# Kernel optimization log

Hardware: AMD Instinct MI355X
Metric: run time of the kernel (lower is better)

## Reference

```python
import jax, jax.numpy as jnp
import numpy as np

B, N, IN, E, H, F = 64, 256, 128, 256, 8, 1024


def setup_inputs() -> dict:
    key = jax.random.key(0)
    ks = jax.random.split(key, 16)
    x = jax.random.normal(ks[0], (B, N, IN), jnp.float32)
    adj = (jax.random.uniform(ks[1], (B, N, N)) < 0.1).astype(jnp.float32)
    adj = jnp.maximum(adj, adj.transpose(0, 2, 1))  # symmetric 0/1 adjacency
    mask = jax.random.randint(ks[2], (B, N), 0, 2).astype(jnp.float32)
    dist = jax.random.normal(ks[3], (B, N, N), jnp.float32)

    def lin(k, i, o):
        return (jax.random.normal(k, (i, o), jnp.float32) / np.sqrt(i)).astype(jnp.float32)

    return dict(
        x=x, adj=adj, mask=mask, dist=dist,
        W1=lin(ks[4], IN, E), b1=jnp.zeros((E,), jnp.float32),
        W2=lin(ks[5], E, E), b2=jnp.zeros((E,), jnp.float32),
        W3=lin(ks[6], E, E), b3=jnp.zeros((E,), jnp.float32),
        ln1_g=jnp.ones((E,), jnp.float32), ln1_b=jnp.zeros((E,), jnp.float32),
        Wq=lin(ks[7], E, H * E), Wk=lin(ks[8], E, H * E), Wv=lin(ks[9], E, H * E),
        Wo=lin(ks[10], H * E, E), bo=jnp.zeros((E,), jnp.float32),
        ln2_g=jnp.ones((E,), jnp.float32), ln2_b=jnp.zeros((E,), jnp.float32),
        Wf1=lin(ks[11], E, F), bf1=jnp.zeros((F,), jnp.float32),
        Wf2=lin(ks[12], F, E), bf2=jnp.zeros((E,), jnp.float32),
    )


def _layernorm(x, g, b):
    m = x.mean(-1, keepdims=True)
    v = ((x - m) ** 2).mean(-1, keepdims=True)
    return (x - m) * jax.lax.rsqrt(v + 1e-5) * g + b


def reference(x, adj, mask, dist, W1, b1, W2, b2, W3, b3, ln1_g, ln1_b,
              Wq, Wk, Wv, Wo, bo, ln2_g, ln2_b, Wf1, bf1, Wf2, bf2):
    # --- DenseGCNConv normalization (add self-loops, sym-normalize) ---
    eye = jnp.eye(N, dtype=adj.dtype)
    A = adj * (1.0 - eye) + eye                      # fill_diag(adj, 1)
    dis = jax.lax.rsqrt(jnp.clip(A.sum(-1), 1.0, None))
    An = dis[:, :, None] * A * dis[:, None, :]       # D^-1/2 A D^-1/2, [B,N,N]
    m3 = mask[:, :, None]

    def gcn(h, W, b):
        return (jnp.einsum('bij,bjf->bif', An, h @ W) + b) * m3

    g1 = jax.nn.relu(gcn(x, W1, b1))
    g2 = jax.nn.relu(gcn(g1, W2, b2))
    g3 = jax.nn.relu(gcn(g2, W3, b3))
    gcn_res = g1 + g2 + g3

    # --- masked MHA with distance bias (head dim = E per head) ---
    h = _layernorm(gcn_res, ln1_g, ln1_b)
    mh = mask[:, None, :, None]                      # [B,1,N,1]
    q = (h @ Wq).reshape(B, N, H, E).transpose(0, 2, 1, 3) * mh
    k = (h @ Wk).reshape(B, N, H, E).transpose(0, 2, 1, 3) * mh
    v = (h @ Wv).reshape(B, N, H, E).transpose(0, 2, 1, 3) * mh
    a = jnp.einsum('bhne,bhme->bhnm', q * (E ** -0.5), k) + dist[:, None]
    am = (mask[:, :, None] * mask[:, None, :])[:, None]  # [B,1,N,N]
    a = jnp.where(am == 0, -1e9, a)
    a = jax.nn.softmax(a, axis=-1)
    a = jnp.where(am == 0, 0.0, a)
    y = jnp.einsum('bhnm,bhme->bhne', a, v).transpose(0, 2, 1, 3).reshape(B, N, H * E)
    y = (y @ Wo + bo) * m3
    att = gcn_res + y

    # --- FFN block ---
    f = _layernorm(att, ln2_g, ln2_b)
    f = (jax.nn.gelu(f @ Wf1 + bf1, approximate=False) @ Wf2 + bf2) * m3
    att = att + f
    return gcn_res + att
```

## Files before the change

kernel.cpp:

```cpp
#include <hip/hip_runtime.h>
#include <hip/hip_bf16.h>
#include <cmath>

#define BB 64
#define NNODES 256
#define INF_ 128
#define EE 256
#define HH 8
#define FFN 1024
#define BNROWS 16384

typedef __attribute__((ext_vector_type(8))) short short8;
typedef __attribute__((ext_vector_type(4))) float floatx4;
typedef __attribute__((ext_vector_type(4))) unsigned short ushort4v;

__device__ __forceinline__ float b2f(unsigned short u) {
  union { unsigned u32; float f; } w; w.u32 = ((unsigned)u) << 16; return w.f;
}
__device__ __forceinline__ unsigned short f2b(float f) {
  union { float f; unsigned u32; } w; w.f = f;
  unsigned r = w.u32 + 0x7FFFu + ((w.u32 >> 16) & 1u);
  return (unsigned short)(r >> 16);
}
__device__ __forceinline__ float gelu_f(float x) {
  const float z = 0.7978845608028654f * (x + 0.044715f * x * x * x);
  const float e = __expf(2.0f * z);
  const float th = (e - 1.0f) / (e + 1.0f);
  return 0.5f * x * (1.0f + th);
}

typedef const __attribute__((address_space(1))) void GV;
typedef __attribute__((address_space(3))) void LV;

__device__ __forceinline__ void gl_lds16(const unsigned short* g,
                                         unsigned short* l, int lane) {
#if __has_builtin(__builtin_amdgcn_global_load_lds)
  __builtin_amdgcn_global_load_lds((GV*)g, (LV*)l, 16, 0, 0);
#else
  *(short8*)(l + lane * 8) = *(const short8*)g;
#endif
}

struct PackArgs {
  const float* src[12];
  unsigned short* dst[12];
  int R[12], C[12];
  int start[13];
};

__launch_bounds__(256)
__global__ void pack_kernel(PackArgs a)
{
  __shared__ float tile[32][33];
  const int bid = blockIdx.x;
  int j = 0;
  while (bid >= a.start[j + 1]) j++;
  const int lb = bid - a.start[j];
  const float* src = a.src[j];
  unsigned short* dst = a.dst[j];
  const int R = a.R[j], C = a.C[j];

  if (C == 0) {
    const int i = (lb * 256 + threadIdx.x) * 4;
    if (i >= R) return;
    floatx4 v = *(const floatx4*)(src + i);
    ushort4v o;
    #pragma unroll
    for (int k = 0; k < 4; k++) o[k] = f2b(v[k]);
    *(ushort4v*)(dst + i) = o;
    return;
  }
  const int tpr = C >> 5;
  const int c0 = (lb % tpr) * 32, r0 = (lb / tpr) * 32;
  const int tx = threadIdx.x & 31, ty = threadIdx.x >> 5;
  #pragma unroll
  for (int i = ty; i < 32; i += 8)
    tile[i][tx] = src[(long long)(r0 + i) * C + c0 + tx];
  __syncthreads();
  #pragma unroll
  for (int i = ty; i < 32; i += 8)
    dst[(long long)(c0 + i) * R + r0 + tx] = f2b(tile[tx][i]);
}

__global__ void deg_kernel(const float* __restrict__ adj,
                           float* __restrict__ dis)
{
  const int g = blockIdx.x * 4 + (threadIdx.x >> 6);
  const int lane = threadIdx.x & 63;
  const int i = g & 255;
  floatx4 v = *(const floatx4*)(adj + (long long)g * 256 + lane * 4);
  float s = 0.f;
  #pragma unroll
  for (int jj = 0; jj < 4; jj++) {
    const int j = lane * 4 + jj;
    s += (j == i) ? 1.0f : v[jj];
  }
  #pragma unroll
  for (int off = 32; off > 0; off >>= 1) s += __shfl_xor(s, off);
  if (lane == 0) dis[g] = 1.0f / sqrtf(fmaxf(s, 1.0f));
}

__global__ void an_kernel(const float* __restrict__ adj,
                          const float* __restrict__ dis,
                          unsigned short* __restrict__ An)
{
  const long long base = ((long long)blockIdx.x * 256 + threadIdx.x) * 4;
  const int rowg = (int)(base >> 8);
  const int i = rowg & 255;
  const int brow = rowg & ~255;
  const int j0 = (int)(base & 255);
  const float di = dis[rowg];
  floatx4 v = *(const floatx4*)(adj + base);
  ushort4v o;
  #pragma unroll
  for (int jj = 0; jj < 4; jj++) {
    const int j = j0 + jj;
    const float a = (j == i) ? 1.0f : v[jj];
    o[jj] = f2b(di * dis[brow + j] * a);
  }
  *(ushort4v*)(An + base) = o;
}

__launch_bounds__(512, 4)
__global__ void gemm_kernel(const unsigned short* __restrict__ A, int lda,
                            long long sAo, long long sAi,
                            const unsigned short* __restrict__ Bm, int ldb,
                            long long sBo, long long sBi,
                            void* __restrict__ Cv, int ldc,
                            long long sCo, long long sCi,
                            int K, int zshift, int mode, int flag,
                            const float* __restrict__ aux1,
                            const float* __restrict__ mask,
                            float* __restrict__ gcn,
                            void* __restrict__ aux2)
{
  __shared__ __align__(16) unsigned short sA[16384];
  __shared__ __align__(16) unsigned short sB[16384];

  const int t = threadIdx.x;
  const int z = blockIdx.z;
  const int zi = z & ((1 << zshift) - 1);
  const int zb = z >> zshift;
  const int m0 = blockIdx.x * 128;
  const int n0 = blockIdx.y * 128;
  A  += zb * sAo + zi * sAi;
  Bm += zb * sBo + zi * sBi;
  const long long cbase = zb * sCo + zi * sCi;

  const int lane = t & 63;
  const int w = t >> 6;
  const int wm = w >> 2, wn = w & 3;
  const int lm = lane & 15, qd = lane >> 4;

  floatx4 acc[4][2] = {};

  const int sub = lane >> 4;
  const int qs  = lane & 15;
  const unsigned short* pA[4];
  const unsigned short* pB[4];
  #pragma unroll
  for (int i = 0; i < 4; i++) {
    const int d = w * 4 + i;
    const int r = d * 4 + sub;
    const int co = (qs ^ (r & 7)) * 8;
    pA[i] = A + (long long)(m0 + r) * lda + co;
    pB[i] = Bm + (long long)(n0 + r) * ldb + co;
  }

  for (int kk = 0; kk < K; kk += 128) {
    #pragma unroll
    for (int i = 0; i < 4; i++) {
      gl_lds16(pA[i] + kk, &sA[(w * 4 + i) * 512], lane);
      gl_lds16(pB[i] + kk, &sB[(w * 4 + i) * 512], lane);
    }
    __syncthreads();

    #pragma unroll
    for (int ks = 0; ks < 4; ks++) {
      short8 af[4], bg[2];
      const int q = ks * 4 + qd;
      #pragma unroll
      for (int mi = 0; mi < 4; mi++) {
        const int r = wm * 64 + mi * 16 + lm;
        af[mi] = *(const short8*)&sA[r * 128 + ((q ^ (r & 7)) * 8)];
      }
      #pragma unroll
      for (int ni = 0; ni < 2; ni++) {
        const int r = wn * 32 + ni * 16 + lm;
        bg[ni] = *(const short8*)&sB[r * 128 + ((q ^ (r & 7)) * 8)];
      }
      #pragma unroll
      for (int mi = 0; mi < 4; mi++)
        #pragma unroll
        for (int ni = 0; ni < 2; ni++)
          acc[mi][ni] = __builtin_amdgcn_mfma_f32_16x16x32_bf16(
              af[mi], bg[ni], acc[mi][ni], 0, 0, 0);
    }
    __syncthreads();
  }

  #pragma unroll
  for (int mi = 0; mi < 4; mi++) {
    const int row0 = m0 + wm * 64 + mi * 16 + qd * 4;
    #pragma unroll
    for (int ni = 0; ni < 2; ni++) {
      const int col = n0 + wn * 32 + ni * 16 + lm;
      floatx4 a = acc[mi][ni];
      if (mode == 0) {
        float* Cf = (float*)Cv;
        #pragma unroll
        for (int r = 0; r < 4; r++)
          Cf[cbase + (long long)(row0 + r) * ldc + col] = a[r];
      } else if (mode == 1) {
        unsigned short* Cb = (unsigned short*)Cv;
        #pragma unroll
        for (int r = 0; r < 4; r++)
          Cb[cbase + (long long)(row0 + r) * ldc + col] = f2b(a[r]);
      } else if (mode == 2) {
        float* Cf = (float*)Cv;
        #pragma unroll
        for (int r = 0; r < 4; r++)
          Cf[cbase + (long long)(row0 + r) * ldc + col] += a[r];
      } else if (mode == 3) {
        unsigned short* Cb = (unsigned short*)Cv;
        const float bv = aux1[col];
        #pragma unroll
        for (int r = 0; r < 4; r++)
          Cb[cbase + (long long)(row0 + r) * ldc + col] = f2b(gelu_f(a[r] + bv));
      } else if (mode == 5) {
        const int b = row0 >> 8, n = row0 & 255;
        ushort4v o;
        #pragma unroll
        for (int r = 0; r < 4; r++) o[r] = f2b(a[r]);
        *(ushort4v*)((unsigned short*)Cv + (long long)b * 65536 + col * 256 + n) = o;
      } else if (mode == 8) {
        float* Cf = (float*)Cv;
        const float* attf = (const float*)aux2;
        const float bv = aux1[col];
        #pragma unroll
        for (int r = 0; r < 4; r++) {
          const long long idx = (long long)(row0 + r) * 256 + col;
          Cf[idx] = gcn[idx] + attf[idx] + (a[r] + bv) * mask[row0 + r];
        }
      } else if (mode == 9) {
        const int token = zb * 256 + col;
        const float m = mask[token];
        ushort4v o; floatx4 g;
        #pragma unroll
        for (int r = 0; r < 4; r++) {
          const float v = fmaxf((a[r] + aux1[row0 + r]) * m, 0.f);
          o[r] = f2b(v); g[r] = v;
        }
        *(ushort4v*)((unsigned short*)Cv + (long long)token * 256 + row0) = o;
        float* gp = gcn + (long long)token * 256 + row0;
        if (flag) { floatx4 old = *(const floatx4*)gp; g += old; }
        *(floatx4*)gp = g;
      } else if (mode == 12) {
        float* Cf = (float*)Cv;
        const float bv = aux1[col];
        #pragma unroll
        for (int r = 0; r < 4; r++) {
          const long long idx = (long long)(row0 + r) * 256 + col;
          Cf[idx] = gcn[idx] + (a[r] + bv) * mask[row0 + r];
        }
      } else if (mode == 13) {
        unsigned short* Cb = (unsigned short*)Cv;
        #pragma unroll
        for (int r = 0; r < 4; r++)
          Cb[cbase + (long long)(row0 + r) * ldc + col] = f2b(a[r] * 0.0625f);
      } else {
        if (col < 2048) {
          unsigned short* Cb = (unsigned short*)Cv;
          #pragma unroll
          for (int r = 0; r < 4; r++)
            Cb[(long long)(row0 + r) * 2048 + col] = f2b(a[r]);
        } else {
          const int z2 = (row0 >> 8) * 8 + ((col >> 8) - 8);
          const int e = col & 255, n = row0 & 255;
          ushort4v o;
          #pragma unroll
          for (int r = 0; r < 4; r++) o[r] = f2b(a[r]);
          *(ushort4v*)((unsigned short*)aux2 + (long long)z2 * 65536 + e * 256 + n) = o;
        }
      }
    }
  }
}

__launch_bounds__(512, 2)
__global__ void attn_kernel(unsigned short* __restrict__ QP,
                            const unsigned short* __restrict__ HBF,
                            const unsigned short* __restrict__ VT,
                            const unsigned short* __restrict__ DSTB,
                            const float* __restrict__ mask)
{
  __shared__ __align__(16) unsigned short sP[32768];
  __shared__ __align__(16) unsigned short sKV[32768];
  __shared__ float redm[2][128];
  __shared__ float reds[2][128];

  const int bi = blockIdx.x;
  const int x = bi & 7, sdx = bi >> 3;
  const int h = sdx & 7;
  const int p = (sdx >> 3) * 8 + x;
  const int b = p >> 1, mt = p & 1;
  const int m0 = mt * 128;
  const int z = b * 8 + h;

  const int t = threadIdx.x, lane = t & 63, w = t >> 6;
  const int lm = lane & 15, qd = lane >> 4;
  const int wm4 = w >> 1, wn2 = w & 1;
  const int wmP = w >> 2, wnP = w & 3;

  unsigned short* Qm = QP + ((long long)(b * 256 + m0)) * 2048 + h * 256;
  const unsigned short* Hb = HBF + (long long)b * 65536;
  const unsigned short* Vb = VT + (long long)z * 65536;
  const unsigned short* db = DSTB + (long long)b * 65536;
  const float* maskb = mask + b * 256;

  const int rin2 = lane >> 5, qs32 = lane & 31;
  const int rin8 = lane >> 3, qs8  = lane & 7;

  #pragma unroll
  for (int i = 0; i < 8; i++) {
    const int d = w * 8 + i;
    const int r = d * 2 + rin2;
    gl_lds16(Qm + (long long)r * 2048 + ((qs32 ^ (r & 7)) * 8), &sP[d * 512], lane);
  }
  #pragma unroll
  for (int i = 0; i < 4; i++) {
    const int d = w * 4 + i;
    const int r = d * 2 + rin2;
    gl_lds16(Hb + (long long)r * 256 + ((qs32 ^ (r & 7)) * 8), &sKV[d * 512], lane);
  }
  __syncthreads();

  short8 afq[2][8];
  #pragma unroll
  for (int mi = 0; mi < 2; mi++) {
    const int r = wm4 * 32 + mi * 16 + lm;
    #pragma unroll
    for (int ks = 0; ks < 8; ks++) {
      const int q = ks * 4 + qd;
      afq[mi][ks] = *(const short8*)&sP[r * 256 + ((q ^ (r & 7)) * 8)];
    }
  }

  floatx4 S[4][2][2] = {};
  #pragma unroll
  for (int c = 0; c < 4; c++) {
    const int cur = (c & 1) * 16384;
    if (c < 3) {
      #pragma unroll
      for (int i = 0; i < 4; i++) {
        const int d = w * 4 + i;
        const int r = d * 2 + rin2;
        gl_lds16(Hb + (long long)((c + 1) * 64 + r) * 256 + ((qs32 ^ (r & 7)) * 8),
                 &sKV[(cur ^ 16384) + d * 512], lane);
      }
    }
    #pragma unroll
    for (int ks = 0; ks < 8; ks++) {
      const int q = ks * 4 + qd;
      short8 bg[2];
      #pragma unroll
      for (int ni = 0; ni < 2; ni++) {
        const int kk = wn2 * 32 + ni * 16 + lm;
        bg[ni] = *(const short8*)&sKV[cur + kk * 256 + ((q ^ (kk & 7)) * 8)];
      }
      #pragma unroll
      for (int mi = 0; mi < 2; mi++)
        #pragma unroll
        for (int ni = 0; ni < 2; ni++)
          S[c][mi][ni] = __builtin_amdgcn_mfma_f32_16x16x32_bf16(
              afq[mi][ks], bg[ni], S[c][mi][ni], 0, 0, 0);
    }
    __syncthreads();
  }

  #pragma unroll
  for (int i = 0; i < 4; i++) {
    const int d = w * 4 + i;
    const int r = d * 8 + rin8;
    gl_lds16(Vb + (long long)r * 256 + ((qs8 ^ (r & 7)) * 8), &sKV[d * 512], lane);
  }

  float mkv[4][2];
  #pragma unroll
  for (int c = 0; c < 4; c++)
    #pragma unroll
    for (int ni = 0; ni < 2; ni++)
      mkv[c][ni] = maskb[c * 64 + wn2 * 32 + ni * 16 + lm];

  float lred[2][4];
  #pragma unroll
  for (int mi = 0; mi < 2; mi++) {
    #pragma unroll
    for (int r = 0; r < 4; r++) {
      const int row = wm4 * 32 + mi * 16 + qd * 4 + r;
      const float mq = maskb[m0 + row];
      float mx = -3e38f;
      #pragma unroll
      for (int c = 0; c < 4; c++)
        #pragma unroll
        for (int ni = 0; ni < 2; ni++) {
          const int col = c * 64 + wn2 * 32 + ni * 16 + lm;
          const float dv = b2f(db[(long long)(m0 + row) * 256 + col]);
          const float v = (mq != 0.f && mkv[c][ni] != 0.f) ? (S[c][mi][ni][r] + dv) : -1e9f;
          S[c][mi][ni][r] = v;
          mx = fmaxf(mx, v);
        }
      lred[mi][r] = mx;
    }
  }
  #pragma unroll
  for (int off = 1; off < 16; off <<= 1)
    #pragma unroll
    for (int mi = 0; mi < 2; mi++)
      #pragma unroll
      for (int r = 0; r < 4; r++)
        lred[mi][r] = fmaxf(lred[mi][r], __shfl_xor(lred[mi][r], off));
  if (lm == 0)
    #pragma unroll
    for (int mi = 0; mi < 2; mi++)
      #pragma unroll
      for (int r = 0; r < 4; r++)
        redm[wn2][wm4 * 32 + mi * 16 + qd * 4 + r] = lred[mi][r];
  __syncthreads();

  #pragma unroll
  for (int mi = 0; mi < 2; mi++) {
    #pragma unroll
    for (int r = 0; r < 4; r++) {
      const int row = wm4 * 32 + mi * 16 + qd * 4 + r;
      const float gmax = fmaxf(redm[0][row], redm[1][row]);
      float ss = 0.f;
      #pragma unroll
      for (int c = 0; c < 4; c++)
        #pragma unroll
        for (int ni = 0; ni < 2; ni++) {
          const float e = __expf(S[c][mi][ni][r] - gmax);
          S[c][mi][ni][r] = e;
          ss += e;
        }
      lred[mi][r] = ss;
    }
  }
  #pragma unroll
  for (int off = 1; off < 16; off <<= 1)
    #pragma unroll
    for (int mi = 0; mi < 2; mi++)
      #pragma unroll
      for (int r = 0; r < 4; r++)
        lred[mi][r] += __shfl_xor(lred[mi][r], off);
  if (lm == 0)
    #pragma unroll
    for (int mi = 0; mi < 2; mi++)
      #pragma unroll
      for (int r = 0; r < 4; r++)
        reds[wn2][wm4 * 32 + mi * 16 + qd * 4 + r] = lred[mi][r];
  __syncthreads();

  #pragma unroll
  for (int mi = 0; mi < 2; mi++)
    #pragma unroll
    for (int r = 0; r < 4; r++) {
      const int row = wm4 * 32 + mi * 16 + qd * 4 + r;
      const float inv = 1.0f / (reds[0][row] + reds[1][row]);
      #pragma unroll
      for (int c = 0; c < 4; c++)
        #pragma unroll
        for (int ni = 0; ni < 2; ni++) {
          const int col = c * 64 + wn2 * 32 + ni * 16 + lm;
          sP[row * 256 + (((col >> 3) ^ (row & 7)) * 8) + (col & 7)] =
              f2b(S[c][mi][ni][r] * inv);
        }
    }
  __syncthreads();

  floatx4 Y[4][4] = {};
  #pragma unroll
  for (int c = 0; c < 4; c++) {
    const int cur = (c & 1) * 16384;
    if (c < 3) {
      #pragma unroll
      for (int i = 0; i < 4; i++) {
        const int d = w * 4 + i;
        const int r = d * 8 + rin8;
        gl_lds16(Vb + (long long)r * 256 + (c + 1) * 64 + ((qs8 ^ (r & 7)) * 8),
                 &sKV[(cur ^ 16384) + d * 512], lane);
      }
    }
    #pragma unroll
    for (int ks = 0; ks < 2; ks++) {
      const int o = ks * 4 + qd;
      const int qP = c * 8 + o;
      short8 af[4], bg[4];
      #pragma unroll
      for (int mi = 0; mi < 4; mi++) {
        const int r = wmP * 64 + mi * 16 + lm;
        af[mi] = *(const short8*)&sP[r * 256 + ((qP ^ (r & 7)) * 8)];
      }
      #pragma unroll
      for (int ni = 0; ni < 4; ni++) {
        const int e = wnP * 64 + ni * 16 + lm;
        bg[ni] = *(const short8*)&sKV[cur + e * 64 + ((o ^ (e & 7)) * 8)];
      }
      #pragma unroll
      for (int mi = 0; mi < 4; mi++)
        #pragma unroll
        for (int ni = 0; ni < 4; ni++)
          Y[mi][ni] = __builtin_amdgcn_mfma_f32_16x16x32_bf16(
              af[mi], bg[ni], Y[mi][ni], 0, 0, 0);
    }
    __syncthreads();
  }

  #pragma unroll
  for (int half = 0; half < 2; half++) {
    __syncthreads();
    if (wmP == half) {
      #pragma unroll
      for (int mi = 0; mi < 4; mi++)
        #pragma unroll
        for (int ni = 0; ni < 4; ni++) {
          const int col = wnP * 64 + ni * 16 + lm;
          #pragma unroll
          for (int r = 0; r < 4; r++) {
            const int rl = mi * 16 + qd * 4 + r;
            sKV[rl * 264 + col] = f2b(Y[mi][ni][r]);
          }
        }
    }
    __syncthreads();
    #pragma unroll
    for (int it = 0; it < 4; it++) {
      const int idx = it * 512 + t;
      const int row = idx >> 5, u = idx & 31;
      short8 v = *(const short8*)&sKV[row * 264 + u * 8];
      *(short8*)(Qm + (long long)(half * 64 + row) * 2048 + u * 8) = v;
    }
  }
}

__global__ void ln_kernel(const float* __restrict__ X,
                          const float* __restrict__ gam,
                          const float* __restrict__ bet,
                          unsigned short* __restrict__ out)
{
  const int g = blockIdx.x * 4 + (threadIdx.x >> 6);
  const int lane = threadIdx.x & 63;
  floatx4 v = *(const floatx4*)(X + (long long)g * 256 + lane * 4);
  float s = v[0] + v[1] + v[2] + v[3];
  float sq = v[0]*v[0] + v[1]*v[1] + v[2]*v[2] + v[3]*v[3];
  #pragma unroll
  for (int off = 32; off > 0; off >>= 1) {
    s  += __shfl_xor(s, off);
    sq += __shfl_xor(sq, off);
  }
  const float mean = s * (1.0f / 256.0f);
  const float var = sq * (1.0f / 256.0f) - mean * mean;
  const float rs = 1.0f / sqrtf(var + 1e-5f);
  ushort4v o;
  #pragma unroll
  for (int jj = 0; jj < 4; jj++) {
    const int c = lane * 4 + jj;
    o[jj] = f2b((v[jj] - mean) * rs * gam[c] + bet[c]);
  }
  *(ushort4v*)(out + (long long)g * 256 + lane * 4) = o;
}

static inline void launch_gemm(hipStream_t st, int M, int N, int batch,
    const void* A, int lda, long long sAo, long long sAi,
    const void* B, int ldb, long long sBo, long long sBi,
    void* C, int ldc, long long sCo, long long sCi,
    int K, int zshift, int mode, int flag,
    const float* aux1, const float* mask, float* gcn, void* aux2)
{
  dim3 grid(M / 128, N / 128, batch), blk(512);
  gemm_kernel<<<grid, blk, 0, st>>>(
      (const unsigned short*)A, lda, sAo, sAi,
      (const unsigned short*)B, ldb, sBo, sBi,
      C, ldc, sCo, sCi, K, zshift, mode, flag, aux1, mask, gcn, aux2);
}

extern "C" void kernel_launch(void* const* d_in, const int* in_sizes, int n_in,
                              void* d_out, int out_size, void* d_ws, size_t ws_size,
                              hipStream_t stream)
{
  (void)in_sizes; (void)n_in; (void)out_size;
  const float* x    = (const float*)d_in[0];
  const float* adj  = (const float*)d_in[1];
  const float* mask = (const float*)d_in[2];
  const float* dist = (const float*)d_in[3];
  const float* W1   = (const float*)d_in[4];
  const float* b1   = (const float*)d_in[5];
  const float* W2   = (const float*)d_in[6];
  const float* b2   = (const float*)d_in[7];
  const float* W3   = (const float*)d_in[8];
  const float* b3   = (const float*)d_in[9];
  const float* ln1g = (const float*)d_in[10];
  const float* ln1b = (const float*)d_in[11];
  const float* Wq   = (const float*)d_in[12];
  const float* Wk   = (const float*)d_in[13];
  const float* Wv   = (const float*)d_in[14];
  const float* Wo   = (const float*)d_in[15];
  const float* bo   = (const float*)d_in[16];
  const float* ln2g = (const float*)d_in[17];
  const float* ln2b = (const float*)d_in[18];
  const float* Wf1  = (const float*)d_in[19];
  const float* bf1  = (const float*)d_in[20];
  const float* Wf2  = (const float*)d_in[21];
  const float* bf2  = (const float*)d_in[22];

  char* w = (char*)d_ws;
  auto alloc = [&](size_t sz) { void* p = (void*)w; w += sz; return p; };
  unsigned short* W1T   = (unsigned short*)alloc(65536);
  unsigned short* W2T   = (unsigned short*)alloc(131072);
  unsigned short* W3T   = (unsigned short*)alloc(131072);
  unsigned short* ABH   = (unsigned short*)alloc(1048576);
  unsigned short* WVT   = (unsigned short*)alloc(1048576);
  unsigned short* WOT   = (unsigned short*)alloc(1048576);
  unsigned short* WF1T  = (unsigned short*)alloc(524288);
  unsigned short* WF2T  = (unsigned short*)alloc(524288);
  unsigned short* WQb   = (unsigned short*)alloc(1048576);
  unsigned short* WKb   = (unsigned short*)alloc(1048576);
  unsigned short* XBF   = (unsigned short*)alloc(4194304);
  unsigned short* DSTB  = (unsigned short*)alloc(8388608);
  float*          GCN   = (float*)         alloc(16777216);
  float*          U     = (float*)         alloc(16777216);
  unsigned short* HBF   = (unsigned short*)alloc(8388608);
  float*          DIS   = (float*)         alloc(65536);
  char* scratch = (char*)alloc(134217728);
  if ((size_t)(w - (char*)d_ws) > ws_size) return;
  unsigned short* AN  = (unsigned short*)scratch;
  unsigned short* TT  = (unsigned short*)(scratch + 8388608);
  unsigned short* GBF = (unsigned short*)(scratch + 16777216);
  unsigned short* QPB = (unsigned short*)scratch;
  unsigned short* VT  = (unsigned short*)(scratch + 67108864);
  unsigned short* FFB = (unsigned short*)scratch;

  PackArgs pa;
  const float* srcs[11] = {W1, W2, W3, Wv, Wo, Wf1, Wf2, x, Wq, Wk, dist};
  unsigned short* dsts[11] = {W1T, W2T, W3T, WVT, WOT, WF1T, WF2T, XBF, WQb, WKb, DSTB};
  const int Rs[11] = {128, 256, 256, 256, 2048, 256, 1024,
                      BNROWS * INF_, EE * HH * EE, EE * HH * EE, BB * 65536};
  const int Cs[11] = {256, 256, 256, 2048, 256, 1024, 256, 0, 0, 0, 0};
  const int sts[12] = {0, 32, 96, 160, 672, 1184, 1440, 1696, 3744, 4256, 4768, 8864};
  for (int j = 0; j < 11; j++) {
    pa.src[j] = srcs[j]; pa.dst[j] = dsts[j]; pa.R[j] = Rs[j]; pa.C[j] = Cs[j];
  }
  for (int j = 0; j < 12; j++) pa.start[j] = sts[j];
  pack_kernel<<<8864, 256, 0, stream>>>(pa);

  deg_kernel<<<4096, 256, 0, stream>>>(adj, DIS);
  an_kernel<<<4096, 256, 0, stream>>>(adj, DIS, AN);

  launch_gemm(stream, 256, 256, 8, WKb, 2048, 256, 0, WQb, 2048, 256, 0,
              ABH, 256, 65536, 0, 256, 0, 13, 0, nullptr, nullptr, nullptr, nullptr);

  launch_gemm(stream, BNROWS, EE, 1, XBF, 128, 0,0, W1T, 128, 0,0,
              TT, 256, 0,0, 128, 0, 5, 0, nullptr, nullptr, nullptr, nullptr);
  launch_gemm(stream, 256, 256, BB, TT, 256, 65536,0, AN, 256, 65536,0,
              GBF, 256, 0,0, 256, 0, 9, 0, b1, mask, GCN, nullptr);
  launch_gemm(stream, BNROWS, EE, 1, GBF, 256, 0,0, W2T, 256, 0,0,
              TT, 256, 0,0, 256, 0, 5, 0, nullptr, nullptr, nullptr, nullptr);
  launch_gemm(stream, 256, 256, BB, TT, 256, 65536,0, AN, 256, 65536,0,
              GBF, 256, 0,0, 256, 0, 9, 1, b2, mask, GCN, nullptr);
  launch_gemm(stream, BNROWS, EE, 1, GBF, 256, 0,0, W3T, 256, 0,0,
              TT, 256, 0,0, 256, 0, 5, 0, nullptr, nullptr, nullptr, nullptr);
  launch_gemm(stream, 256, 256, BB, TT, 256, 65536,0, AN, 256, 65536,0,
              GBF, 256, 0,0, 256, 0, 9, 1, b3, mask, GCN, nullptr);

  ln_kernel<<<4096, 256, 0, stream>>>(GCN, ln1g, ln1b, HBF);

  launch_gemm(stream, BNROWS, 4096, 1, HBF, 256, 0,0, ABH, 256, 0,0,
              QPB, 2048, 0,0, 256, 0, 15, 0, nullptr, nullptr, nullptr, VT);
  attn_kernel<<<1024, 512, 0, stream>>>(QPB, HBF, VT, DSTB, mask);
  launch_gemm(stream, BNROWS, EE, 1, QPB, 2048, 0,0, WOT, 2048, 0,0,
              U, 256, 0,0, 2048, 0, 12, 0, bo, mask, GCN, nullptr);

  ln_kernel<<<4096, 256, 0, stream>>>(U, ln2g, ln2b, HBF);
  launch_gemm(stream, BNROWS, FFN, 1, HBF, 256, 0,0, WF1T, 256, 0,0,
              FFB, 1024, 0,0, 256, 0, 3, 0, bf1, nullptr, nullptr, nullptr);
  launch_gemm(stream, BNROWS, EE, 1, FFB, 1024, 0,0, WF2T, 1024, 0,0,
              d_out, 256, 0,0, 1024, 0, 8, 0, bf2, mask, GCN, U);
}
```

Before: 478.2 us.

## Split attention into 64-row query tiles with smaller LDS for higher occupancy

The attention kernel now handles 64 query rows per block instead of 128, so twice as many blocks are launched, and shared memory is roughly halved to allow four blocks per CU. The K and V tiles are single-buffered with a barrier after each refill, replacing the previous double-buffered prefetch. The distance bias is loaded straight into the score accumulators before the QK matmul, and s_setprio is raised around the MFMA loops. The trade-off is more synchronisation, lost load/compute overlap inside a block, and the H rows (keys) being reloaded by twice as many blocks.

```diff
diff --git a/kernel.cpp b/kernel.cpp
--- a/kernel.cpp
+++ b/kernel.cpp
@@ -287,95 +287,102 @@
   }
 }
 
-__launch_bounds__(512, 2)
+__launch_bounds__(512, 4)
 __global__ void attn_kernel(unsigned short* __restrict__ QP,
                             const unsigned short* __restrict__ HBF,
                             const unsigned short* __restrict__ VT,
                             const unsigned short* __restrict__ DSTB,
                             const float* __restrict__ mask)
 {
-  __shared__ __align__(16) unsigned short sP[32768];
-  __shared__ __align__(16) unsigned short sKV[32768];
-  __shared__ float redm[2][128];
-  __shared__ float reds[2][128];
+  __shared__ __align__(16) unsigned short sP[16896];
+  __shared__ __align__(16) unsigned short sKV[16384];
+  __shared__ float redm[4][64];
+  __shared__ float reds[4][64];
 
   const int bi = blockIdx.x;
-  const int x = bi & 7, sdx = bi >> 3;
-  const int h = sdx & 7;
-  const int p = (sdx >> 3) * 8 + x;
-  const int b = p >> 1, mt = p & 1;
-  const int m0 = mt * 128;
+  const int x = bi & 7;
+  const int h = (bi >> 3) & 7;
+  const int p = (bi >> 6) * 8 + x;
+  const int b = p >> 2, mt = p & 3;
+  const int m0 = mt * 64;
   const int z = b * 8 + h;
 
   const int t = threadIdx.x, lane = t & 63, w = t >> 6;
   const int lm = lane & 15, qd = lane >> 4;
-  const int wm4 = w >> 1, wn2 = w & 1;
-  const int wmP = w >> 2, wnP = w & 3;
+  const int wm2 = w >> 2, wn4 = w & 3;
 
   unsigned short* Qm = QP + ((long long)(b * 256 + m0)) * 2048 + h * 256;
   const unsigned short* Hb = HBF + (long long)b * 65536;
   const unsigned short* Vb = VT + (long long)z * 65536;
-  const unsigned short* db = DSTB + (long long)b * 65536;
+  const unsigned short* db = DSTB + (long long)b * 65536 + (long long)m0 * 256;
   const float* maskb = mask + b * 256;
 
   const int rin2 = lane >> 5, qs32 = lane & 31;
   const int rin8 = lane >> 3, qs8  = lane & 7;
 
-  #pragma unroll
-  for (int i = 0; i < 8; i++) {
-    const int d = w * 8 + i;
-    const int r = d * 2 + rin2;
-    gl_lds16(Qm + (long long)r * 2048 + ((qs32 ^ (r & 7)) * 8), &sP[d * 512], lane);
-  }
+  floatx4 S[2][4];
+  #pragma unroll
+  for (int mi = 0; mi < 2; mi++)
+    #pragma unroll
+    for (int ni = 0; ni < 4; ni++) {
+      const int col = wn4 * 64 + ni * 16 + lm;
+      #pragma unroll
+      for (int r = 0; r < 4; r++) {
+        const int row = wm2 * 32 + mi * 16 + qd * 4 + r;
+        S[mi][ni][r] = b2f(db[row * 256 + col]);
+      }
+    }
+
   #pragma unroll
   for (int i = 0; i < 4; i++) {
     const int d = w * 4 + i;
     const int r = d * 2 + rin2;
-    gl_lds16(Hb + (long long)r * 256 + ((qs32 ^ (r & 7)) * 8), &sKV[d * 512], lane);
+    gl_lds16(Qm + (long long)r * 2048 + ((qs32 ^ (r & 7)) * 8), &sP[d * 512], lane);
+  }
+  #pragma unroll
+  for (int i = 0; i < 4; i++) {
+    const int d = w * 4 + i;
+    const int r = d * 8 + rin8;
+    gl_lds16(Hb + (long long)r * 256 + ((qs8 ^ (r & 7)) * 8), &sKV[d * 512], lane);
   }
   __syncthreads();
 
-  short8 afq[2][8];
-  #pragma unroll
-  for (int mi = 0; mi < 2; mi++) {
-    const int r = wm4 * 32 + mi * 16 + lm;
-    #pragma unroll
-    for (int ks = 0; ks < 8; ks++) {
-      const int q = ks * 4 + qd;
-      afq[mi][ks] = *(const short8*)&sP[r * 256 + ((q ^ (r & 7)) * 8)];
-    }
-  }
-
-  floatx4 S[4][2][2] = {};
-  #pragma unroll
   for (int c = 0; c < 4; c++) {
-    const int cur = (c & 1) * 16384;
+    __builtin_amdgcn_s_setprio(1);
+    #pragma unroll
+    for (int ks = 0; ks < 2; ks++) {
+      const int ol = ks * 4 + qd;
+      short8 af[2], bg[4];
+      #pragma unroll
+      for (int mi = 0; mi < 2; mi++) {
+        const int r = wm2 * 32 + mi * 16 + lm;
+        const int q = c * 8 + ol;
+        af[mi] = *(const short8*)&sP[r * 256 + ((q ^ (r & 7)) * 8)];
+      }
+      #pragma unroll
+      for (int ni = 0; ni < 4; ni++) {
+        const int kk = wn4 * 64 + ni * 16 + lm;
+        bg[ni] = *(const short8*)&sKV[kk * 64 + ((ol ^ (kk & 7)) * 8)];
+      }
+      #pragma unroll
+      for (int mi = 0; mi < 2; mi++)
+        #pragma unroll
+        for (int ni = 0; ni < 4; ni++)
+          S[mi][ni] = __builtin_amdgcn_mfma_f32_16x16x32_bf16(
+              af[mi], bg[ni], S[mi][ni], 0, 0, 0);
+    }
+    __builtin_amdgcn_s_setprio(0);
+    __syncthreads();
     if (c < 3) {
       #pragma unroll
       for (int i = 0; i < 4; i++) {
         const int d = w * 4 + i;
-        const int r = d * 2 + rin2;
-        gl_lds16(Hb + (long long)((c + 1) * 64 + r) * 256 + ((qs32 ^ (r & 7)) * 8),
-                 &sKV[(cur ^ 16384) + d * 512], lane);
-      }
-    }
-    #pragma unroll
-    for (int ks = 0; ks < 8; ks++) {
-      const int q = ks * 4 + qd;
-      short8 bg[2];
-      #pragma unroll
-      for (int ni = 0; ni < 2; ni++) {
-        const int kk = wn2 * 32 + ni * 16 + lm;
-        bg[ni] = *(const short8*)&sKV[cur + kk * 256 + ((q ^ (kk & 7)) * 8)];
-      }
-      #pragma unroll
-      for (int mi = 0; mi < 2; mi++)
-        #pragma unroll
-        for (int ni = 0; ni < 2; ni++)
-          S[c][mi][ni] = __builtin_amdgcn_mfma_f32_16x16x32_bf16(
-              afq[mi][ks], bg[ni], S[c][mi][ni], 0, 0, 0);
-    }
-    __syncthreads();
+        const int r = d * 8 + rin8;
+        gl_lds16(Hb + (long long)r * 256 + (c + 1) * 64 + ((qs8 ^ (r & 7)) * 8),
+                 &sKV[d * 512], lane);
+      }
+      __syncthreads();
+    }
   }
 
   #pragma unroll
@@ -385,31 +392,24 @@
     gl_lds16(Vb + (long long)r * 256 + ((qs8 ^ (r & 7)) * 8), &sKV[d * 512], lane);
   }
 
-  float mkv[4][2];
-  #pragma unroll
-  for (int c = 0; c < 4; c++)
-    #pragma unroll
-    for (int ni = 0; ni < 2; ni++)
-      mkv[c][ni] = maskb[c * 64 + wn2 * 32 + ni * 16 + lm];
+  float mkv[4];
+  #pragma unroll
+  for (int ni = 0; ni < 4; ni++) mkv[ni] = maskb[wn4 * 64 + ni * 16 + lm];
 
   float lred[2][4];
   #pragma unroll
   for (int mi = 0; mi < 2; mi++) {
     #pragma unroll
     for (int r = 0; r < 4; r++) {
-      const int row = wm4 * 32 + mi * 16 + qd * 4 + r;
+      const int row = wm2 * 32 + mi * 16 + qd * 4 + r;
       const float mq = maskb[m0 + row];
       float mx = -3e38f;
       #pragma unroll
-      for (int c = 0; c < 4; c++)
-        #pragma unroll
-        for (int ni = 0; ni < 2; ni++) {
-          const int col = c * 64 + wn2 * 32 + ni * 16 + lm;
-          const float dv = b2f(db[(long long)(m0 + row) * 256 + col]);
-          const float v = (mq != 0.f && mkv[c][ni] != 0.f) ? (S[c][mi][ni][r] + dv) : -1e9f;
-          S[c][mi][ni][r] = v;
-          mx = fmaxf(mx, v);
-        }
+      for (int ni = 0; ni < 4; ni++) {
+        const float v = (mq != 0.f && mkv[ni] != 0.f) ? S[mi][ni][r] : -1e9f;
+        S[mi][ni][r] = v;
+        mx = fmaxf(mx, v);
+      }
       lred[mi][r] = mx;
     }
   }
@@ -425,24 +425,23 @@
     for (int mi = 0; mi < 2; mi++)
       #pragma unroll
       for (int r = 0; r < 4; r++)
-        redm[wn2][wm4 * 32 + mi * 16 + qd * 4 + r] = lred[mi][r];
+        redm[wn4][wm2 * 32 + mi * 16 + qd * 4 + r] = lred[mi][r];
   __syncthreads();
 
   #pragma unroll
   for (int mi = 0; mi < 2; mi++) {
     #pragma unroll
     for (int r = 0; r < 4; r++) {
-      const int row = wm4 * 32 + mi * 16 + qd * 4 + r;
-      const float gmax = fmaxf(redm[0][row], redm[1][row]);
+      const int row = wm2 * 32 + mi * 16 + qd * 4 + r;
+      const float gmax = fmaxf(fmaxf(redm[0][row], redm[1][row]),
+                               fmaxf(redm[2][row], redm[3][row]));
       float ss = 0.f;
       #pragma unroll
-      for (int c = 0; c < 4; c++)
-        #pragma unroll
-        for (int ni = 0; ni < 2; ni++) {
-          const float e = __expf(S[c][mi][ni][r] - gmax);
-          S[c][mi][ni][r] = e;
-          ss += e;
-        }
+      for (int ni = 0; ni < 4; ni++) {
+        const float e = __expf(S[mi][ni][r] - gmax);
+        S[mi][ni][r] = e;
+        ss += e;
+      }
       lred[mi][r] = ss;
     }
   }
@@ -458,88 +457,82 @@
     for (int mi = 0; mi < 2; mi++)
       #pragma unroll
       for (int r = 0; r < 4; r++)
-        reds[wn2][wm4 * 32 + mi * 16 + qd * 4 + r] = lred[mi][r];
+        reds[wn4][wm2 * 32 + mi * 16 + qd * 4 + r] = lred[mi][r];
   __syncthreads();
 
   #pragma unroll
   for (int mi = 0; mi < 2; mi++)
     #pragma unroll
     for (int r = 0; r < 4; r++) {
-      const int row = wm4 * 32 + mi * 16 + qd * 4 + r;
-      const float inv = 1.0f / (reds[0][row] + reds[1][row]);
-      #pragma unroll
-      for (int c = 0; c < 4; c++)
-        #pragma unroll
-        for (int ni = 0; ni < 2; ni++) {
-          const int col = c * 64 + wn2 * 32 + ni * 16 + lm;
-          sP[row * 256 + (((col >> 3) ^ (row & 7)) * 8) + (col & 7)] =
-              f2b(S[c][mi][ni][r] * inv);
-        }
+      const int row = wm2 * 32 + mi * 16 + qd * 4 + r;
+      const float inv = 1.0f / (reds[0][row] + reds[1][row] +
+                                reds[2][row] + reds[3][row]);
+      #pragma unroll
+      for (int ni = 0; ni < 4; ni++) {
+        const int kl = ni * 16 + lm;
+        const int slot = (kl >> 3) ^ (row & 7);
+        sP[wn4 * 4096 + row * 64 + slot * 8 + (kl & 7)] =
+            f2b(S[mi][ni][r] * inv);
+      }
     }
   __syncthreads();
 
-  floatx4 Y[4][4] = {};
-  #pragma unroll
+  floatx4 Y[2][4] = {};
   for (int c = 0; c < 4; c++) {
-    const int cur = (c & 1) * 16384;
+    __builtin_amdgcn_s_setprio(1);
+    #pragma unroll
+    for (int ks = 0; ks < 2; ks++) {
+      const int ol = ks * 4 + qd;
+      short8 af[2], bg[4];
+      #pragma unroll
+      for (int mi = 0; mi < 2; mi++) {
+        const int r = wm2 * 32 + mi * 16 + lm;
+        af[mi] = *(const short8*)&sP[c * 4096 + r * 64 + ((ol ^ (r & 7)) * 8)];
+      }
+      #pragma unroll
+      for (int ni = 0; ni < 4; ni++) {
+        const int ee = wn4 * 64 + ni * 16 + lm;
+        bg[ni] = *(const short8*)&sKV[ee * 64 + ((ol ^ (ee & 7)) * 8)];
+      }
+      #pragma unroll
+      for (int mi = 0; mi < 2; mi++)
+        #pragma unroll
+        for (int ni = 0; ni < 4; ni++)
+          Y[mi][ni] = __builtin_amdgcn_mfma_f32_16x16x32_bf16(
+              af[mi], bg[ni], Y[mi][ni], 0, 0, 0);
+    }
+    __builtin_amdgcn_s_setprio(0);
+    __syncthreads();
     if (c < 3) {
       #pragma unroll
       for (int i = 0; i < 4; i++) {
         const int d = w * 4 + i;
         const int r = d * 8 + rin8;
         gl_lds16(Vb + (long long)r * 256 + (c + 1) * 64 + ((qs8 ^ (r & 7)) * 8),
-                 &sKV[(cur ^ 16384) + d * 512], lane);
-      }
-    }
-    #pragma unroll
-    for (int ks = 0; ks < 2; ks++) {
-      const int o = ks * 4 + qd;
-      const int qP = c * 8 + o;
-      short8 af[4], bg[4];
-      #pragma unroll
-      for (int mi = 0; mi < 4; mi++) {
-        const int r = wmP * 64 + mi * 16 + lm;
-        af[mi] = *(const short8*)&sP[r * 256 + ((qP ^ (r & 7)) * 8)];
-      }
-      #pragma unroll
-      for (int ni = 0; ni < 4; ni++) {
-        const int e = wnP * 64 + ni * 16 + lm;
-        bg[ni] = *(const short8*)&sKV[cur + e * 64 + ((o ^ (e & 7)) * 8)];
-      }
-      #pragma unroll
-      for (int mi = 0; mi < 4; mi++)
-        #pragma unroll
-        for (int ni = 0; ni < 4; ni++)
-          Y[mi][ni] = __builtin_amdgcn_mfma_f32_16x16x32_bf16(
-              af[mi], bg[ni], Y[mi][ni], 0, 0, 0);
-    }
-    __syncthreads();
-  }
-
-  #pragma unroll
-  for (int half = 0; half < 2; half++) {
-    __syncthreads();
-    if (wmP == half) {
-      #pragma unroll
-      for (int mi = 0; mi < 4; mi++)
-        #pragma unroll
-        for (int ni = 0; ni < 4; ni++) {
-          const int col = wnP * 64 + ni * 16 + lm;
-          #pragma unroll
-          for (int r = 0; r < 4; r++) {
-            const int rl = mi * 16 + qd * 4 + r;
-            sKV[rl * 264 + col] = f2b(Y[mi][ni][r]);
-          }
-        }
-    }
-    __syncthreads();
-    #pragma unroll
-    for (int it = 0; it < 4; it++) {
-      const int idx = it * 512 + t;
-      const int row = idx >> 5, u = idx & 31;
-      short8 v = *(const short8*)&sKV[row * 264 + u * 8];
-      *(short8*)(Qm + (long long)(half * 64 + row) * 2048 + u * 8) = v;
-    }
+                 &sKV[d * 512], lane);
+      }
+      __syncthreads();
+    }
+  }
+
+  #pragma unroll
+  for (int mi = 0; mi < 2; mi++)
+    #pragma unroll
+    for (int ni = 0; ni < 4; ni++) {
+      const int col = wn4 * 64 + ni * 16 + lm;
+      #pragma unroll
+      for (int r = 0; r < 4; r++) {
+        const int rl = wm2 * 32 + mi * 16 + qd * 4 + r;
+        sP[rl * 264 + col] = f2b(Y[mi][ni][r]);
+      }
+    }
+  __syncthreads();
+  #pragma unroll
+  for (int it = 0; it < 4; it++) {
+    const int idx = it * 512 + t;
+    const int row = idx >> 5, u = idx & 31;
+    short8 v = *(const short8*)&sP[row * 264 + u * 8];
+    *(short8*)(Qm + (long long)row * 2048 + u * 8) = v;
   }
 }
 
@@ -676,7 +669,7 @@
 
   launch_gemm(stream, BNROWS, 4096, 1, HBF, 256, 0,0, ABH, 256, 0,0,
               QPB, 2048, 0,0, 256, 0, 15, 0, nullptr, nullptr, nullptr, VT);
-  attn_kernel<<<1024, 512, 0, stream>>>(QPB, HBF, VT, DSTB, mask);
+  attn_kernel<<<2048, 512, 0, stream>>>(QPB, HBF, VT, DSTB, mask);
   launch_gemm(stream, BNROWS, EE, 1, QPB, 2048, 0,0, WOT, 2048, 0,0,
               U, 256, 0,0, 2048, 0, 12, 0, bo, mask, GCN, nullptr);
 
```

Result: faster. 467.4 us (-2.3%).
